# Kernel optimization log

Measured on AMD Instinct MI355X. Metric: run time of the kernel, lower is better.

## Reference

```python
import jax, jax.numpy as jnp
import numpy as np

B, T, N, H = 16, 49, 24, 256
S = 0.05  # init scale (keeps sigmoids/tanh out of saturation for numeric testing)


def setup_inputs() -> dict:
    key = jax.random.key(0)
    ks = jax.random.split(key, 16)
    rn = lambda k, shp: (jax.random.normal(k, shp, dtype=jnp.float32) * S)
    return dict(
        h=rn(ks[0], (B, T, N, H)),
        c_h=rn(ks[1], (B, T, N, H)),
        p=rn(ks[2], (B, T, N, H)),
        g_t=rn(ks[3], (B, T, N, H)),
        c_g_t=rn(ks[4], (B, T, N, H)),
        g_s=rn(ks[5], (B, T, N, H)),
        c_g_s=rn(ks[6], (B, T, N, H)),
        # 9 h-gates stacked in order: i, lt, ft, rt, s, gt, gs, o, c
        U=rn(ks[7], (9, N, H, H)),
        Wt=rn(ks[8], (9, N, 3 * H, H)),
        Ws=rn(ks[9], (9, N, H, H)),
        Zt=rn(ks[10], (9, N, H, H)),
        Zs=rn(ks[11], (9, N, H, H)),
        b=rn(ks[12], (9, N, 1, H)),
        # 6 global gates stacked in order: gtf, gtg, gto, gsf, gsg, gso
        Wg=rn(ks[13], (6, N, H, H)),
        Zg=rn(ks[14], (6, N, H, H)),
        bg=rn(ks[15], (6, N, 1, H)),
        train=1,
    )


def _cell(h, c_h, p, g_t, c_g_t, g_s, c_g_s, U, Wt, Ws, Zt, Zs, b, Wg, Zg, bg):
    pad_t = jnp.zeros_like(h[:, :, :1, :])
    pad_s = jnp.zeros_like(h[:, :1, :, :])
    # spatial (bone) neighbours along axis 2
    h_t_before = jnp.concatenate([pad_t, h[:, :, :-1, :]], axis=2)
    h_t_after = jnp.concatenate([h[:, :, 1:, :], pad_t], axis=2)
    h_tba = jnp.concatenate([h_t_before, h, h_t_after], axis=3)  # [B,T,N,3H]
    c_t_before = jnp.concatenate([pad_t, c_h[:, :, :-1, :]], axis=2)
    c_t_after = jnp.concatenate([c_h[:, :, 1:, :], pad_t], axis=2)
    # temporal predecessor along axis 1
    h_s_before = jnp.concatenate([pad_s, h[:, :-1, :, :]], axis=1)
    c_s_before = jnp.concatenate([pad_s, c_h[:, :-1, :, :]], axis=1)

    # Faithful quirk of the source: f_ft gate uses Zslt (the lt gate's Zs) for its g_s term.
    Zs_eff = Zs.at[2].set(Zs[1])

    # All 9 gate preactivations in one fused batched-GEMM pass: [9,B,T,N,H]
    pre = (jnp.einsum('btnh,gnhk->gbtnk', p, U)
           + jnp.einsum('btnm,gnmk->gbtnk', h_tba, Wt)
           + jnp.einsum('btnh,gnhk->gbtnk', h_s_before, Ws)
           + jnp.einsum('btnh,gnhk->gbtnk', g_t, Zt)
           + jnp.einsum('btnh,gnhk->gbtnk', g_s, Zs_eff)
           + b[:, None, None, :, 0, :])
    i_n, f_lt, f_ft, f_rt, f_s, f_gt, f_gs, o_n = jax.nn.sigmoid(pre[:8])
    c_n = jnp.tanh(pre[8])

    c_h_new = (f_lt * c_t_before + f_ft * c_h + f_rt * c_t_after
               + f_s * c_s_before + f_gt * c_g_t + f_gs * c_g_s + i_n * c_n)
    h_new = o_n * jnp.tanh(c_h_new)

    def _global(x_g, c_g, Wg3, Zg3, bg3):
        pre_g = (jnp.einsum('btnh,gnhk->gbtnk', h_new, Wg3)
                 + jnp.einsum('btnh,gnhk->gbtnk', x_g, Zg3)
                 + bg3[:, None, None, :, 0, :])
        f_g = jax.nn.sigmoid(pre_g[0])
        cand = jnp.tanh(pre_g[1])
        o_g = jax.nn.sigmoid(pre_g[2])
        c_g_new = f_g * c_g + (1.0 - f_g) * cand
        return o_g * jnp.tanh(c_g_new), c_g_new

    g_t_new, c_g_t_new = _global(g_t, c_g_t, Wg[:3], Zg[:3], bg[:3])
    g_s_new, c_g_s_new = _global(g_s, c_g_s, Wg[3:], Zg[3:], bg[3:])
    return h_new, c_h_new, g_t_new, c_g_t_new, g_s_new, c_g_s_new


def reference(h, c_h, p, g_t, c_g_t, g_s, c_g_s, U, Wt, Ws, Zt, Zs, b, Wg, Zg, bg, train):
    # `train` is a flag unused by the cell's math (kept for signature fidelity)
    return _cell(h, c_h, p, g_t, c_g_t, g_s, c_g_s, U, Wt, Ws, Zt, Zs, b, Wg, Zg, bg)
```

## Files before the change

### kernel.cpp

```cpp
#include <hip/hip_runtime.h>
#include <hip/hip_bf16.h>

typedef unsigned short u16;
typedef u16 u16x8 __attribute__((ext_vector_type(8)));
typedef short s16x8 __attribute__((ext_vector_type(8)));
typedef float f32x4 __attribute__((ext_vector_type(4)));
typedef unsigned int u32;

#define NN 24
#define TT 49
#define MR 784
#define SZT 4816896

__device__ inline u16 f2b(float f){
    __hip_bfloat16 b = __float2bfloat16(f); u16 r; __builtin_memcpy(&r, &b, 2); return r;
}
__device__ inline float sig_(float x){ return 1.f / (1.f + __expf(-x)); }
__device__ inline float tanh_(float x){ float e = __expf(2.f * x); return (e - 1.f) / (e + 1.f); }

__device__ inline void gld16(const u16* g, u16* l){
    __builtin_amdgcn_global_load_lds(
        (const __attribute__((address_space(1))) unsigned int*)g,
        (__attribute__((address_space(3))) unsigned int*)l, 16, 0, 0);
}

#define WT0_ELEMS ((size_t)216 * 256 * 1792)
#define WT1_ELEMS ((size_t)144 * 256 * 512)

__global__ __launch_bounds__(256) void wprep0(
    const float* __restrict__ U,  const float* __restrict__ Wt,
    const float* __restrict__ Ws, const float* __restrict__ Zt,
    const float* __restrict__ Zs, u16* __restrict__ out)
{
    __shared__ u16 T[64][72];
    const int tid = threadIdx.x;
    const int kt = blockIdx.x, ct = blockIdx.y, z = blockIdx.z;
    const int n = z % NN, g = z / NN;
    const int k0 = kt * 64;

    const float* wbase;
    if (k0 < 256)       wbase = U  + (size_t)((g * NN + n) * 256 + k0)          * 256;
    else if (k0 < 1024) wbase = Wt + (size_t)((g * NN + n) * 768 + (k0 - 256))  * 256;
    else if (k0 < 1280) wbase = Ws + (size_t)((g * NN + n) * 256 + (k0 - 1024)) * 256;
    else if (k0 < 1536) wbase = Zt + (size_t)((g * NN + n) * 256 + (k0 - 1280)) * 256;
    else { const int g2 = (g == 2) ? 1 : g;
           wbase = Zs + (size_t)((g2 * NN + n) * 256 + (k0 - 1536)) * 256; }

    const int colg = ct * 64 + (tid & 15) * 4;
    #pragma unroll
    for (int it = 0; it < 4; ++it) {
        const int krl = (tid >> 4) + it * 16;
        const float4 v = *(const float4*)(wbase + (size_t)krl * 256 + colg);
        const int cl = (tid & 15) * 4;
        T[cl + 0][krl] = f2b(v.x); T[cl + 1][krl] = f2b(v.y);
        T[cl + 2][krl] = f2b(v.z); T[cl + 3][krl] = f2b(v.w);
    }
    __syncthreads();
    const int col_l = tid >> 2, ks = (tid & 3) * 16;
    const int ktile = 2 * kt + (ks >> 5);
    const int koff  = ks & 31;
    u16* dst = out + (size_t)z * 458752 + (size_t)ktile * 8192
                   + (size_t)(ct * 64 + col_l) * 32 + koff;
    u16x8 w0, w1;
    #pragma unroll
    for (int j = 0; j < 8; ++j) { w0[j] = T[col_l][ks + j]; w1[j] = T[col_l][ks + 8 + j]; }
    *(u16x8*)(dst) = w0; *(u16x8*)(dst + 8) = w1;
}

__global__ __launch_bounds__(256) void wprep1(
    const float* __restrict__ Wg, const float* __restrict__ Zg, u16* __restrict__ out)
{
    __shared__ u16 T[64][72];
    const int tid = threadIdx.x;
    const int kt = blockIdx.x, ct = blockIdx.y, z = blockIdx.z;
    const int k0 = kt * 64;
    const float* wbase = (k0 < 256)
        ? Wg + (size_t)(z * 256 + k0) * 256
        : Zg + (size_t)(z * 256 + (k0 - 256)) * 256;

    const int colg = ct * 64 + (tid & 15) * 4;
    #pragma unroll
    for (int it = 0; it < 4; ++it) {
        const int krl = (tid >> 4) + it * 16;
        const float4 v = *(const float4*)(wbase + (size_t)krl * 256 + colg);
        const int cl = (tid & 15) * 4;
        T[cl + 0][krl] = f2b(v.x); T[cl + 1][krl] = f2b(v.y);
        T[cl + 2][krl] = f2b(v.z); T[cl + 3][krl] = f2b(v.w);
    }
    __syncthreads();
    const int col_l = tid >> 2, ks = (tid & 3) * 16;
    const int ktile = 2 * kt + (ks >> 5);
    const int koff  = ks & 31;
    u16* dst = out + (size_t)z * 131072 + (size_t)ktile * 8192
                   + (size_t)(ct * 64 + col_l) * 32 + koff;
    u16x8 w0, w1;
    #pragma unroll
    for (int j = 0; j < 8; ++j) { w0[j] = T[col_l][ks + j]; w1[j] = T[col_l][ks + 8 + j]; }
    *(u16x8*)(dst) = w0; *(u16x8*)(dst + 8) = w1;
}

#define AB2 2048
#define BB2 18432

__global__ __launch_bounds__(256, 2) void fused_cell4(
    const float* __restrict__ p,   const float* __restrict__ h,
    const float* __restrict__ c_h, const float* __restrict__ g_t,
    const float* __restrict__ c_g_t, const float* __restrict__ g_s,
    const float* __restrict__ c_g_s,
    const u16* __restrict__ WT0, const float* __restrict__ Bias,
    float* __restrict__ h_new, float* __restrict__ c_h_new)
{
    extern __shared__ u16 smem[];

    const int tid = threadIdx.x;
    const int lin = blockIdx.x;
    const int xcd = lin & 7, j = lin >> 3;
    const int mtile = j % 13;
    const int slab  = (j / 13) * 8 + xcd;
    const int ntile = slab & 3, n = slab >> 2;

    const int s_r = tid >> 2, s_c = tid & 3;
    const int gr  = mtile * 64 + s_r;
    const bool mval = (gr < MR);
    const int ec = (gr * NN + n) * 256;
    const bool vnb = (n > 0), vna = (n < NN - 1), vtp = (gr % TT) != 0;

    const int wro = s_r * 32 + ((s_c ^ ((s_r >> 1) & 3)) << 3);

    const int wave = tid >> 6, lane = tid & 63;
    const int lrow = lane & 15, lci = lane >> 4;

    int aro[4];
    #pragma unroll
    for (int m = 0; m < 4; ++m) {
        const int row = m * 16 + lrow;
        aro[m] = row * 32 + ((lci ^ ((row >> 1) & 3)) << 3);
    }
    const int colr = wave * 16 + lrow;
    const int bro  = colr * 32 + ((lci ^ ((colr >> 1) & 3)) << 3);

    const size_t bsrc = (size_t)(ntile * 64) * 32 + (size_t)wro;
    const u16* wbase = WT0 + (size_t)n * 458752 + bsrc;

    f32x4 acc[9][4];
    #pragma unroll
    for (int g = 0; g < 9; ++g)
        #pragma unroll
        for (int m = 0; m < 4; ++m) acc[g][m] = f32x4{0.f, 0.f, 0.f, 0.f};

    float4 alo, ahi;

    auto loadA = [&](int kt) {
        const int K0 = kt * 32, seg = K0 >> 8, koff = (K0 & 255) + s_c * 8;
        const float* src = nullptr; bool valid = mval;
        switch (seg) {
            case 0: src = p + ec + koff; break;
            case 1: valid &= vnb; src = h + ec - 256 + koff; break;
            case 2: src = h + ec + koff; break;
            case 3: valid &= vna; src = h + ec + 256 + koff; break;
            case 4: valid &= vtp; src = h + ec - NN * 256 + koff; break;
            case 5: src = g_t + ec + koff; break;
            default: src = g_s + ec + koff; break;
        }
        alo = make_float4(0.f, 0.f, 0.f, 0.f); ahi = alo;
        if (valid) { alo = *(const float4*)src; ahi = *(const float4*)(src + 4); }
    };
    auto storeA = [&](int buf) {
        u16x8 aw;
        aw[0] = f2b(alo.x); aw[1] = f2b(alo.y); aw[2] = f2b(alo.z); aw[3] = f2b(alo.w);
        aw[4] = f2b(ahi.x); aw[5] = f2b(ahi.y); aw[6] = f2b(ahi.z); aw[7] = f2b(ahi.w);
        *(u16x8*)(&smem[buf * AB2 + wro]) = aw;
    };
    auto dmaB = [&](int kt, int buf) {
        const u16* wb = wbase + (size_t)kt * 8192;
        u16* dst = &smem[2 * AB2 + buf * BB2 + tid * 8];
        #pragma unroll
        for (int g = 0; g < 9; ++g)
            gld16(wb + (size_t)g * 11010048, dst + g * 2048);
    };
    auto domfma = [&](int buf) {
        const u16* Asb = smem + buf * AB2;
        const u16* Bsb = smem + 2 * AB2 + buf * BB2;
        s16x8 af[4];
        #pragma unroll
        for (int m = 0; m < 4; ++m) af[m] = *(const s16x8*)(&Asb[aro[m]]);
        __builtin_amdgcn_s_setprio(1);
        #pragma unroll
        for (int g = 0; g < 9; ++g) {
            const s16x8 bf = *(const s16x8*)(&Bsb[g * 2048 + bro]);
            #pragma unroll
            for (int m = 0; m < 4; ++m)
                acc[g][m] = __builtin_amdgcn_mfma_f32_16x16x32_bf16(af[m], bf, acc[g][m], 0, 0, 0);
        }
        __builtin_amdgcn_s_setprio(0);
    };

    dmaB(0, 0); loadA(0); storeA(0);
    for (int kt = 0; kt < 56; kt += 2) {
        __syncthreads();
        dmaB(kt + 1, 1); loadA(kt + 1);
        domfma(0);
        storeA(1);
        __syncthreads();
        if (kt + 2 < 56) { dmaB(kt + 2, 0); loadA(kt + 2); }
        domfma(1);
        if (kt + 2 < 56) storeA(0);
    }

    const int col = ntile * 64 + wave * 16 + lrow;
    float bv[9];
    #pragma unroll
    for (int g = 0; g < 9; ++g) bv[g] = Bias[(g * NN + n) * 256 + col];

    #pragma unroll
    for (int m = 0; m < 4; ++m) {
        #pragma unroll
        for (int i = 0; i < 4; ++i) {
            const int row = mtile * 64 + m * 16 + (lane >> 4) * 4 + i;
            if (row < MR) {
                const size_t e = ((size_t)(row * NN + n)) * 256 + col;
                const float i_n  = sig_(acc[0][m][i] + bv[0]);
                const float f_lt = sig_(acc[1][m][i] + bv[1]);
                const float f_ft = sig_(acc[2][m][i] + bv[2]);
                const float f_rt = sig_(acc[3][m][i] + bv[3]);
                const float f_s  = sig_(acc[4][m][i] + bv[4]);
                const float f_gt = sig_(acc[5][m][i] + bv[5]);
                const float f_gs = sig_(acc[6][m][i] + bv[6]);
                const float o_n  = sig_(acc[7][m][i] + bv[7]);
                const float c_n  = tanh_(acc[8][m][i] + bv[8]);
                const float cb = (n > 0)      ? c_h[e - 256] : 0.f;
                const float ca = (n < NN - 1) ? c_h[e + 256] : 0.f;
                const float cs = (row % TT)   ? c_h[e - NN * 256] : 0.f;
                const float cn = f_lt * cb + f_ft * c_h[e] + f_rt * ca
                               + f_s * cs + f_gt * c_g_t[e] + f_gs * c_g_s[e]
                               + i_n * c_n;
                c_h_new[e] = cn;
                h_new[e]   = o_n * tanh_(cn);
            }
        }
    }
}

__global__ __launch_bounds__(256, 4) void fused_global4(
    const float* __restrict__ hn,   const float* __restrict__ g_t,
    const float* __restrict__ g_s,  const float* __restrict__ c_g_t,
    const float* __restrict__ c_g_s,
    const u16* __restrict__ WT1, const float* __restrict__ Bg,
    float* __restrict__ out2, float* __restrict__ out3,
    float* __restrict__ out4, float* __restrict__ out5)
{
    __shared__ u16 smem[2 * 2048 + 2 * 6144];

    const int tid = threadIdx.x;
    const int lin = blockIdx.x;
    const int xcd = lin & 7, j = lin >> 3;
    const int mtile = j % 13;
    const int slab  = (j / 13) * 8 + xcd;
    const int ntile = slab & 3;
    const int zz    = slab >> 2;
    const int n = zz % NN, grp = zz / NN;

    const float* xg = grp ? g_s : g_t;
    const float* cg = grp ? c_g_s : c_g_t;
    float* og  = grp ? out4 : out2;
    float* ocg = grp ? out5 : out3;

    const int s_r = tid >> 2, s_c = tid & 3;
    const int gr  = mtile * 64 + s_r;
    const bool mval = (gr < MR);
    const int ec = (gr * NN + n) * 256;

    const int wro = s_r * 32 + ((s_c ^ ((s_r >> 1) & 3)) << 3);

    const int wave = tid >> 6, lane = tid & 63;
    const int lrow = lane & 15, lci = lane >> 4;

    int aro[4];
    #pragma unroll
    for (int m = 0; m < 4; ++m) {
        const int row = m * 16 + lrow;
        aro[m] = row * 32 + ((lci ^ ((row >> 1) & 3)) << 3);
    }
    const int colr = wave * 16 + lrow;
    const int bro  = colr * 32 + ((lci ^ ((colr >> 1) & 3)) << 3);

    const size_t bsrc = (size_t)(ntile * 64) * 32 + (size_t)wro;
    const u16* wbase = WT1 + (size_t)(grp * 3 * NN + n) * 131072 + bsrc;

    f32x4 acc[3][4];
    #pragma unroll
    for (int g = 0; g < 3; ++g)
        #pragma unroll
        for (int m = 0; m < 4; ++m) acc[g][m] = f32x4{0.f, 0.f, 0.f, 0.f};

    float4 alo, ahi;

    auto loadA = [&](int kt) {
        const int K0 = kt * 32, koff = (K0 & 255) + s_c * 8;
        const float* src = ((K0 < 256) ? hn : xg) + ec + koff;
        alo = make_float4(0.f, 0.f, 0.f, 0.f); ahi = alo;
        if (mval) { alo = *(const float4*)src; ahi = *(const float4*)(src + 4); }
    };
    auto storeA = [&](int buf) {
        u16x8 aw;
        aw[0] = f2b(alo.x); aw[1] = f2b(alo.y); aw[2] = f2b(alo.z); aw[3] = f2b(alo.w);
        aw[4] = f2b(ahi.x); aw[5] = f2b(ahi.y); aw[6] = f2b(ahi.z); aw[7] = f2b(ahi.w);
        *(u16x8*)(&smem[buf * 2048 + wro]) = aw;
    };
    auto dmaB = [&](int kt, int buf) {
        const u16* wb = wbase + (size_t)kt * 8192;
        u16* dst = &smem[2 * 2048 + buf * 6144 + tid * 8];
        #pragma unroll
        for (int g = 0; g < 3; ++g)
            gld16(wb + (size_t)g * 3145728, dst + g * 2048);
    };
    auto domfma = [&](int buf) {
        const u16* Asb = smem + buf * 2048;
        const u16* Bsb = smem + 2 * 2048 + buf * 6144;
        s16x8 af[4];
        #pragma unroll
        for (int m = 0; m < 4; ++m) af[m] = *(const s16x8*)(&Asb[aro[m]]);
        __builtin_amdgcn_s_setprio(1);
        #pragma unroll
        for (int g = 0; g < 3; ++g) {
            const s16x8 bf = *(const s16x8*)(&Bsb[g * 2048 + bro]);
            #pragma unroll
            for (int m = 0; m < 4; ++m)
                acc[g][m] = __builtin_amdgcn_mfma_f32_16x16x32_bf16(af[m], bf, acc[g][m], 0, 0, 0);
        }
        __builtin_amdgcn_s_setprio(0);
    };

    dmaB(0, 0); loadA(0); storeA(0);
    for (int kt = 0; kt < 16; kt += 2) {
        __syncthreads();
        dmaB(kt + 1, 1); loadA(kt + 1);
        domfma(0);
        storeA(1);
        __syncthreads();
        if (kt + 2 < 16) { dmaB(kt + 2, 0); loadA(kt + 2); }
        domfma(1);
        if (kt + 2 < 16) storeA(0);
    }

    const int col = ntile * 64 + wave * 16 + lrow;
    float bv[3];
    #pragma unroll
    for (int g = 0; g < 3; ++g) bv[g] = Bg[((grp * 3 + g) * NN + n) * 256 + col];

    #pragma unroll
    for (int m = 0; m < 4; ++m) {
        #pragma unroll
        for (int i = 0; i < 4; ++i) {
            const int row = mtile * 64 + m * 16 + (lane >> 4) * 4 + i;
            if (row < MR) {
                const size_t e = ((size_t)(row * NN + n)) * 256 + col;
                const float f    = sig_(acc[0][m][i] + bv[0]);
                const float cand = tanh_(acc[1][m][i] + bv[1]);
                const float o    = sig_(acc[2][m][i] + bv[2]);
                const float cn = f * cg[e] + (1.f - f) * cand;
                ocg[e] = cn;
                og[e]  = o * tanh_(cn);
            }
        }
    }
}

extern "C" void kernel_launch(void* const* d_in, const int* in_sizes, int n_in,
                              void* d_out, int out_size, void* d_ws, size_t ws_size,
                              hipStream_t stream)
{
    const float* h     = (const float*)d_in[0];
    const float* c_h   = (const float*)d_in[1];
    const float* p     = (const float*)d_in[2];
    const float* g_t   = (const float*)d_in[3];
    const float* c_g_t = (const float*)d_in[4];
    const float* g_s   = (const float*)d_in[5];
    const float* c_g_s = (const float*)d_in[6];
    const float* U     = (const float*)d_in[7];
    const float* Wt    = (const float*)d_in[8];
    const float* Ws    = (const float*)d_in[9];
    const float* Zt    = (const float*)d_in[10];
    const float* Zs    = (const float*)d_in[11];
    const float* bb    = (const float*)d_in[12];
    const float* Wg    = (const float*)d_in[13];
    const float* Zg    = (const float*)d_in[14];
    const float* bg    = (const float*)d_in[15];

    float* out0 = (float*)d_out;
    float* out1 = out0 + (size_t)SZT;
    float* out2 = out1 + (size_t)SZT;
    float* out3 = out2 + (size_t)SZT;
    float* out4 = out3 + (size_t)SZT;
    float* out5 = out4 + (size_t)SZT;

    u16* wt0 = (u16*)d_ws;
    u16* wt1 = wt0 + WT0_ELEMS;

    dim3 blk(256);
    wprep0<<<dim3(28, 4, 216), blk, 0, stream>>>(U, Wt, Ws, Zt, Zs, wt0);
    wprep1<<<dim3(8, 4, 144), blk, 0, stream>>>(Wg, Zg, wt1);

    hipFuncSetAttribute((const void*)fused_cell4,
                        hipFuncAttributeMaxDynamicSharedMemorySize, 81920);
    fused_cell4<<<dim3(1248), blk, 81920, stream>>>(
        p, h, c_h, g_t, c_g_t, g_s, c_g_s, wt0, bb, out0, out1);
    fused_global4<<<dim3(2496), blk, 0, stream>>>(
        out0, g_t, g_s, c_g_t, c_g_s, wt1, bg, out2, out3, out4, out5);
}
```

Baseline: 487.9 us.

## Pre-pack activations to bf16 tiles and DMA them directly into LDS

Adds an aprep kernel that gathers the seven concatenated activation segments (p, h neighbours, temporal predecessor, g_t, g_s), converts them to bf16 and writes them in a tile-major layout in the workspace. A new fused_cell5 then streams these A tiles into LDS with global_load_lds, as it already does for weights. This removes the per-tile fp32 loads, conversions and LDS stores from the GEMM main loop, and cuts the A traffic that was reloaded once per column tile. It costs an extra pass that writes and reads a ~34MB bf16 buffer, and it only runs when the workspace is large enough; otherwise the old kernel runs with loads reordered.

```diff
diff --git a/kernel.cpp b/kernel.cpp
--- a/kernel.cpp
+++ b/kernel.cpp
@@ -26,6 +26,9 @@
 
 #define WT0_ELEMS ((size_t)216 * 256 * 1792)
 #define WT1_ELEMS ((size_t)144 * 256 * 512)
+#define ABF_ELEMS ((size_t)24 * 56 * 784 * 32)
+#define NEED_BASE ((WT0_ELEMS + WT1_ELEMS) * 2)
+#define NEED_A    (NEED_BASE + ABF_ELEMS * 2 + 4096)
 
 __global__ __launch_bounds__(256) void wprep0(
     const float* __restrict__ U,  const float* __restrict__ Wt,
@@ -99,15 +102,45 @@
     *(u16x8*)(dst) = w0; *(u16x8*)(dst + 8) = w1;
 }
 
+__global__ __launch_bounds__(256) void aprep(
+    const float* __restrict__ p,   const float* __restrict__ h,
+    const float* __restrict__ g_t, const float* __restrict__ g_s,
+    u16* __restrict__ Abf)
+{
+    const int tid = threadIdx.x;
+    const int bx = blockIdx.x, kt = blockIdx.y, n = blockIdx.z;
+    const int row = bx * 64 + (tid >> 2);
+    if (row >= MR) return;
+    const int c  = tid & 3;
+    const int kg = kt * 32 + c * 8;
+    const int seg = kg >> 8, koff = kg & 255;
+    const int ec = (row * NN + n) * 256 + koff;
+    const float* src = nullptr; bool valid = true;
+    switch (seg) {
+        case 0: src = p + ec; break;
+        case 1: valid = (n > 0);          src = h + ec - 256; break;
+        case 2: src = h + ec; break;
+        case 3: valid = (n < NN - 1);     src = h + ec + 256; break;
+        case 4: valid = (row % TT) != 0;  src = h + ec - NN * 256; break;
+        case 5: src = g_t + ec; break;
+        default: src = g_s + ec; break;
+    }
+    float4 lo = {0.f,0.f,0.f,0.f}, hi = lo;
+    if (valid) { lo = *(const float4*)src; hi = *(const float4*)(src + 4); }
+    u16x8 w;
+    w[0] = f2b(lo.x); w[1] = f2b(lo.y); w[2] = f2b(lo.z); w[3] = f2b(lo.w);
+    w[4] = f2b(hi.x); w[5] = f2b(hi.y); w[6] = f2b(hi.z); w[7] = f2b(hi.w);
+    *(u16x8*)(Abf + ((size_t)(n * 56 + kt) * MR + row) * 32 + c * 8) = w;
+}
+
 #define AB2 2048
 #define BB2 18432
 
-__global__ __launch_bounds__(256, 2) void fused_cell4(
-    const float* __restrict__ p,   const float* __restrict__ h,
-    const float* __restrict__ c_h, const float* __restrict__ g_t,
-    const float* __restrict__ c_g_t, const float* __restrict__ g_s,
+__global__ __launch_bounds__(256, 2) void fused_cell5(
+    const float* __restrict__ c_h, const float* __restrict__ c_g_t,
     const float* __restrict__ c_g_s,
-    const u16* __restrict__ WT0, const float* __restrict__ Bias,
+    const u16* __restrict__ Abf, const u16* __restrict__ WT0,
+    const float* __restrict__ Bias,
     float* __restrict__ h_new, float* __restrict__ c_h_new)
 {
     extern __shared__ u16 smem[];
@@ -120,11 +153,6 @@
     const int ntile = slab & 3, n = slab >> 2;
 
     const int s_r = tid >> 2, s_c = tid & 3;
-    const int gr  = mtile * 64 + s_r;
-    const bool mval = (gr < MR);
-    const int ec = (gr * NN + n) * 256;
-    const bool vnb = (n > 0), vna = (n < NN - 1), vtp = (gr % TT) != 0;
-
     const int wro = s_r * 32 + ((s_c ^ ((s_r >> 1) & 3)) << 3);
 
     const int wave = tid >> 6, lane = tid & 63;
@@ -139,8 +167,8 @@
     const int colr = wave * 16 + lrow;
     const int bro  = colr * 32 + ((lci ^ ((colr >> 1) & 3)) << 3);
 
-    const size_t bsrc = (size_t)(ntile * 64) * 32 + (size_t)wro;
-    const u16* wbase = WT0 + (size_t)n * 458752 + bsrc;
+    const u16* abase = Abf + ((size_t)(n * 56) * MR + mtile * 64) * 32 + wro;
+    const u16* wbase = WT0 + (size_t)n * 458752 + (size_t)(ntile * 64) * 32 + wro;
 
     f32x4 acc[9][4];
     #pragma unroll
@@ -148,30 +176,8 @@
         #pragma unroll
         for (int m = 0; m < 4; ++m) acc[g][m] = f32x4{0.f, 0.f, 0.f, 0.f};
 
-    float4 alo, ahi;
-
-    auto loadA = [&](int kt) {
-        const int K0 = kt * 32, seg = K0 >> 8, koff = (K0 & 255) + s_c * 8;
-        const float* src = nullptr; bool valid = mval;
-        switch (seg) {
-            case 0: src = p + ec + koff; break;
-            case 1: valid &= vnb; src = h + ec - 256 + koff; break;
-            case 2: src = h + ec + koff; break;
-            case 3: valid &= vna; src = h + ec + 256 + koff; break;
-            case 4: valid &= vtp; src = h + ec - NN * 256 + koff; break;
-            case 5: src = g_t + ec + koff; break;
-            default: src = g_s + ec + koff; break;
-        }
-        alo = make_float4(0.f, 0.f, 0.f, 0.f); ahi = alo;
-        if (valid) { alo = *(const float4*)src; ahi = *(const float4*)(src + 4); }
-    };
-    auto storeA = [&](int buf) {
-        u16x8 aw;
-        aw[0] = f2b(alo.x); aw[1] = f2b(alo.y); aw[2] = f2b(alo.z); aw[3] = f2b(alo.w);
-        aw[4] = f2b(ahi.x); aw[5] = f2b(ahi.y); aw[6] = f2b(ahi.z); aw[7] = f2b(ahi.w);
-        *(u16x8*)(&smem[buf * AB2 + wro]) = aw;
-    };
-    auto dmaB = [&](int kt, int buf) {
+    auto dma = [&](int kt, int buf) {
+        gld16(abase + (size_t)kt * (MR * 32), &smem[buf * AB2 + tid * 8]);
         const u16* wb = wbase + (size_t)kt * 8192;
         u16* dst = &smem[2 * AB2 + buf * BB2 + tid * 8];
         #pragma unroll
@@ -195,16 +201,14 @@
         __builtin_amdgcn_s_setprio(0);
     };
 
-    dmaB(0, 0); loadA(0); storeA(0);
+    dma(0, 0);
     for (int kt = 0; kt < 56; kt += 2) {
         __syncthreads();
-        dmaB(kt + 1, 1); loadA(kt + 1);
+        dma(kt + 1, 1);
         domfma(0);
-        storeA(1);
         __syncthreads();
-        if (kt + 2 < 56) { dmaB(kt + 2, 0); loadA(kt + 2); }
+        if (kt + 2 < 56) dma(kt + 2, 0);
         domfma(1);
-        if (kt + 2 < 56) storeA(0);
     }
 
     const int col = ntile * 64 + wave * 16 + lrow;
@@ -241,6 +245,145 @@
     }
 }
 
+__global__ __launch_bounds__(256, 2) void fused_cell4(
+    const float* __restrict__ p,   const float* __restrict__ h,
+    const float* __restrict__ c_h, const float* __restrict__ g_t,
+    const float* __restrict__ c_g_t, const float* __restrict__ g_s,
+    const float* __restrict__ c_g_s,
+    const u16* __restrict__ WT0, const float* __restrict__ Bias,
+    float* __restrict__ h_new, float* __restrict__ c_h_new)
+{
+    extern __shared__ u16 smem[];
+
+    const int tid = threadIdx.x;
+    const int lin = blockIdx.x;
+    const int xcd = lin & 7, j = lin >> 3;
+    const int mtile = j % 13;
+    const int slab  = (j / 13) * 8 + xcd;
+    const int ntile = slab & 3, n = slab >> 2;
+
+    const int s_r = tid >> 2, s_c = tid & 3;
+    const int gr  = mtile * 64 + s_r;
+    const bool mval = (gr < MR);
+    const int ec = (gr * NN + n) * 256;
+    const bool vnb = (n > 0), vna = (n < NN - 1), vtp = (gr % TT) != 0;
+
+    const int wro = s_r * 32 + ((s_c ^ ((s_r >> 1) & 3)) << 3);
+
+    const int wave = tid >> 6, lane = tid & 63;
+    const int lrow = lane & 15, lci = lane >> 4;
+
+    int aro[4];
+    #pragma unroll
+    for (int m = 0; m < 4; ++m) {
+        const int row = m * 16 + lrow;
+        aro[m] = row * 32 + ((lci ^ ((row >> 1) & 3)) << 3);
+    }
+    const int colr = wave * 16 + lrow;
+    const int bro  = colr * 32 + ((lci ^ ((colr >> 1) & 3)) << 3);
+
+    const size_t bsrc = (size_t)(ntile * 64) * 32 + (size_t)wro;
+    const u16* wbase = WT0 + (size_t)n * 458752 + bsrc;
+
+    f32x4 acc[9][4];
+    #pragma unroll
+    for (int g = 0; g < 9; ++g)
+        #pragma unroll
+        for (int m = 0; m < 4; ++m) acc[g][m] = f32x4{0.f, 0.f, 0.f, 0.f};
+
+    float4 alo, ahi;
+
+    auto loadA = [&](int kt) {
+        const int K0 = kt * 32, seg = K0 >> 8, koff = (K0 & 255) + s_c * 8;
+        const float* src = nullptr; bool valid = mval;
+        switch (seg) {
+            case 0: src = p + ec + koff; break;
+            case 1: valid &= vnb; src = h + ec - 256 + koff; break;
+            case 2: src = h + ec + koff; break;
+            case 3: valid &= vna; src = h + ec + 256 + koff; break;
+            case 4: valid &= vtp; src = h + ec - NN * 256 + koff; break;
+            case 5: src = g_t + ec + koff; break;
+            default: src = g_s + ec + koff; break;
+        }
+        alo = make_float4(0.f, 0.f, 0.f, 0.f); ahi = alo;
+        if (valid) { alo = *(const float4*)src; ahi = *(const float4*)(src + 4); }
+    };
+    auto storeA = [&](int buf) {
+        u16x8 aw;
+        aw[0] = f2b(alo.x); aw[1] = f2b(alo.y); aw[2] = f2b(alo.z); aw[3] = f2b(alo.w);
+        aw[4] = f2b(ahi.x); aw[5] = f2b(ahi.y); aw[6] = f2b(ahi.z); aw[7] = f2b(ahi.w);
+        *(u16x8*)(&smem[buf * AB2 + wro]) = aw;
+    };
+    auto dmaB = [&](int kt, int buf) {
+        const u16* wb = wbase + (size_t)kt * 8192;
+        u16* dst = &smem[2 * AB2 + buf * BB2 + tid * 8];
+        #pragma unroll
+        for (int g = 0; g < 9; ++g)
+            gld16(wb + (size_t)g * 11010048, dst + g * 2048);
+    };
+    auto domfma = [&](int buf) {
+        const u16* Asb = smem + buf * AB2;
+        const u16* Bsb = smem + 2 * AB2 + buf * BB2;
+        s16x8 af[4];
+        #pragma unroll
+        for (int m = 0; m < 4; ++m) af[m] = *(const s16x8*)(&Asb[aro[m]]);
+        __builtin_amdgcn_s_setprio(1);
+        #pragma unroll
+        for (int g = 0; g < 9; ++g) {
+            const s16x8 bf = *(const s16x8*)(&Bsb[g * 2048 + bro]);
+            #pragma unroll
+            for (int m = 0; m < 4; ++m)
+                acc[g][m] = __builtin_amdgcn_mfma_f32_16x16x32_bf16(af[m], bf, acc[g][m], 0, 0, 0);
+        }
+        __builtin_amdgcn_s_setprio(0);
+    };
+
+    dmaB(0, 0); loadA(0); storeA(0);
+    for (int kt = 0; kt < 56; kt += 2) {
+        __syncthreads();
+        loadA(kt + 1); dmaB(kt + 1, 1);
+        domfma(0);
+        storeA(1);
+        __syncthreads();
+        if (kt + 2 < 56) { loadA(kt + 2); dmaB(kt + 2, 0); }
+        domfma(1);
+        if (kt + 2 < 56) storeA(0);
+    }
+
+    const int col = ntile * 64 + wave * 16 + lrow;
+    float bv[9];
+    #pragma unroll
+    for (int g = 0; g < 9; ++g) bv[g] = Bias[(g * NN + n) * 256 + col];
+
+    #pragma unroll
+    for (int m = 0; m < 4; ++m) {
+        #pragma unroll
+        for (int i = 0; i < 4; ++i) {
+            const int row = mtile * 64 + m * 16 + (lane >> 4) * 4 + i;
+            if (row < MR) {
+                const size_t e = ((size_t)(row * NN + n)) * 256 + col;
+                const float i_n  = sig_(acc[0][m][i] + bv[0]);
+                const float f_lt = sig_(acc[1][m][i] + bv[1]);
+                const float f_ft = sig_(acc[2][m][i] + bv[2]);
+                const float f_rt = sig_(acc[3][m][i] + bv[3]);
+                const float f_s  = sig_(acc[4][m][i] + bv[4]);
+                const float f_gt = sig_(acc[5][m][i] + bv[5]);
+                const float f_gs = sig_(acc[6][m][i] + bv[6]);
+                const float o_n  = sig_(acc[7][m][i] + bv[7]);
+                const float c_n  = tanh_(acc[8][m][i] + bv[8]);
+                const float cb = (n > 0)      ? c_h[e - 256] : 0.f;
+                const float ca = (n < NN - 1) ? c_h[e + 256] : 0.f;
+                const float cs = (row % TT)   ? c_h[e - NN * 256] : 0.f;
+                const float cn = f_lt * cb + f_ft * c_h[e] + f_rt * ca
+                               + f_s * cs + f_gt * c_g_t[e] + f_gs * c_g_s[e]
+                               + i_n * c_n;
+                c_h_new[e] = cn;
+                h_new[e]   = o_n * tanh_(cn);
+            }
+        }
+    }
+}
+
 __global__ __launch_bounds__(256, 4) void fused_global4(
     const float* __restrict__ hn,   const float* __restrict__ g_t,
     const float* __restrict__ g_s,  const float* __restrict__ c_g_t,
@@ -331,14 +474,14 @@
         __builtin_amdgcn_s_setprio(0);
     };
 
-    dmaB(0, 0); loadA(0); storeA(0);
+    loadA(0); dmaB(0, 0); storeA(0);
     for (int kt = 0; kt < 16; kt += 2) {
         __syncthreads();
-        dmaB(kt + 1, 1); loadA(kt + 1);
+        loadA(kt + 1); dmaB(kt + 1, 1);
         domfma(0);
         storeA(1);
         __syncthreads();
-        if (kt + 2 < 16) { dmaB(kt + 2, 0); loadA(kt + 2); }
+        if (kt + 2 < 16) { loadA(kt + 2); dmaB(kt + 2, 0); }
         domfma(1);
         if (kt + 2 < 16) storeA(0);
     }
@@ -396,15 +539,24 @@
 
     u16* wt0 = (u16*)d_ws;
     u16* wt1 = wt0 + WT0_ELEMS;
+    u16* abf = wt1 + WT1_ELEMS;
 
     dim3 blk(256);
     wprep0<<<dim3(28, 4, 216), blk, 0, stream>>>(U, Wt, Ws, Zt, Zs, wt0);
     wprep1<<<dim3(8, 4, 144), blk, 0, stream>>>(Wg, Zg, wt1);
 
-    hipFuncSetAttribute((const void*)fused_cell4,
-                        hipFuncAttributeMaxDynamicSharedMemorySize, 81920);
-    fused_cell4<<<dim3(1248), blk, 81920, stream>>>(
-        p, h, c_h, g_t, c_g_t, g_s, c_g_s, wt0, bb, out0, out1);
+    if (ws_size >= NEED_A) {
+        aprep<<<dim3(13, 56, 24), blk, 0, stream>>>(p, h, g_t, g_s, abf);
+        hipFuncSetAttribute((const void*)fused_cell5,
+                            hipFuncAttributeMaxDynamicSharedMemorySize, 81920);
+        fused_cell5<<<dim3(1248), blk, 81920, stream>>>(
+            c_h, c_g_t, c_g_s, abf, wt0, bb, out0, out1);
+    } else {
+        hipFuncSetAttribute((const void*)fused_cell4,
+                            hipFuncAttributeMaxDynamicSharedMemorySize, 81920);
+        fused_cell4<<<dim3(1248), blk, 81920, stream>>>(
+            p, h, c_h, g_t, c_g_t, g_s, c_g_s, wt0, bb, out0, out1);
+    }
     fused_global4<<<dim3(2496), blk, 0, stream>>>(
         out0, g_t, g_s, c_g_t, c_g_s, wt1, bg, out2, out3, out4, out5);
 }
```

Measured after the change: 512.4 us. +5.0%, slower.

## Pre-convert activations to bf16 tiles and DMA both operands with explicit waitcnt pipelining

Applied to the files above, without the earlier changes.

The two weight-prep kernels are merged into one prep launch, which also converts the concatenated A operand (p, h neighbours, g_t, g_s) into a bf16 k-tiled buffer in workspace. The main cell GEMM then loads A straight into LDS with global_load_lds alongside B, so the fp32-load, convert and LDS-store work leaves its inner loop. Its loop is restructured around raw s_barrier and vmcnt waits so the next tile's DMA overlaps the current MFMA. The global-gate kernel gets a similar double-register prefetch with explicit waitcnts. In exchange, an extra bf16 activation buffer has to be written and read back, and the hand-tuned waitcnt counts add a correctness risk.

```diff
diff --git a/kernel.cpp b/kernel.cpp
--- a/kernel.cpp
+++ b/kernel.cpp
@@ -24,90 +24,118 @@
         (__attribute__((address_space(3))) unsigned int*)l, 16, 0, 0);
 }
 
+#define BAR()      __builtin_amdgcn_s_barrier()
+#define WAITVM(N)  asm volatile("s_waitcnt vmcnt(" #N ")" ::: "memory")
+#define WAITVL(N)  asm volatile("s_waitcnt vmcnt(" #N ") lgkmcnt(0)" ::: "memory")
+
 #define WT0_ELEMS ((size_t)216 * 256 * 1792)
 #define WT1_ELEMS ((size_t)144 * 256 * 512)
 
-__global__ __launch_bounds__(256) void wprep0(
+__global__ __launch_bounds__(256) void prep_all(
     const float* __restrict__ U,  const float* __restrict__ Wt,
     const float* __restrict__ Ws, const float* __restrict__ Zt,
-    const float* __restrict__ Zs, u16* __restrict__ out)
+    const float* __restrict__ Zs, const float* __restrict__ Wg,
+    const float* __restrict__ Zg,
+    const float* __restrict__ p,  const float* __restrict__ h,
+    const float* __restrict__ g_t, const float* __restrict__ g_s,
+    u16* __restrict__ wt0, u16* __restrict__ wt1, u16* __restrict__ Abf)
 {
     __shared__ u16 T[64][72];
     const int tid = threadIdx.x;
-    const int kt = blockIdx.x, ct = blockIdx.y, z = blockIdx.z;
-    const int n = z % NN, g = z / NN;
-    const int k0 = kt * 64;
-
-    const float* wbase;
-    if (k0 < 256)       wbase = U  + (size_t)((g * NN + n) * 256 + k0)          * 256;
-    else if (k0 < 1024) wbase = Wt + (size_t)((g * NN + n) * 768 + (k0 - 256))  * 256;
-    else if (k0 < 1280) wbase = Ws + (size_t)((g * NN + n) * 256 + (k0 - 1024)) * 256;
-    else if (k0 < 1536) wbase = Zt + (size_t)((g * NN + n) * 256 + (k0 - 1280)) * 256;
-    else { const int g2 = (g == 2) ? 1 : g;
-           wbase = Zs + (size_t)((g2 * NN + n) * 256 + (k0 - 1536)) * 256; }
-
-    const int colg = ct * 64 + (tid & 15) * 4;
-    #pragma unroll
-    for (int it = 0; it < 4; ++it) {
-        const int krl = (tid >> 4) + it * 16;
-        const float4 v = *(const float4*)(wbase + (size_t)krl * 256 + colg);
-        const int cl = (tid & 15) * 4;
-        T[cl + 0][krl] = f2b(v.x); T[cl + 1][krl] = f2b(v.y);
-        T[cl + 2][krl] = f2b(v.z); T[cl + 3][krl] = f2b(v.w);
-    }
-    __syncthreads();
-    const int col_l = tid >> 2, ks = (tid & 3) * 16;
-    const int ktile = 2 * kt + (ks >> 5);
-    const int koff  = ks & 31;
-    u16* dst = out + (size_t)z * 458752 + (size_t)ktile * 8192
-                   + (size_t)(ct * 64 + col_l) * 32 + koff;
-    u16x8 w0, w1;
-    #pragma unroll
-    for (int j = 0; j < 8; ++j) { w0[j] = T[col_l][ks + j]; w1[j] = T[col_l][ks + 8 + j]; }
-    *(u16x8*)(dst) = w0; *(u16x8*)(dst + 8) = w1;
-}
-
-__global__ __launch_bounds__(256) void wprep1(
-    const float* __restrict__ Wg, const float* __restrict__ Zg, u16* __restrict__ out)
-{
-    __shared__ u16 T[64][72];
-    const int tid = threadIdx.x;
-    const int kt = blockIdx.x, ct = blockIdx.y, z = blockIdx.z;
-    const int k0 = kt * 64;
-    const float* wbase = (k0 < 256)
-        ? Wg + (size_t)(z * 256 + k0) * 256
-        : Zg + (size_t)(z * 256 + (k0 - 256)) * 256;
-
-    const int colg = ct * 64 + (tid & 15) * 4;
-    #pragma unroll
-    for (int it = 0; it < 4; ++it) {
-        const int krl = (tid >> 4) + it * 16;
-        const float4 v = *(const float4*)(wbase + (size_t)krl * 256 + colg);
-        const int cl = (tid & 15) * 4;
-        T[cl + 0][krl] = f2b(v.x); T[cl + 1][krl] = f2b(v.y);
-        T[cl + 2][krl] = f2b(v.z); T[cl + 3][krl] = f2b(v.w);
-    }
-    __syncthreads();
-    const int col_l = tid >> 2, ks = (tid & 3) * 16;
-    const int ktile = 2 * kt + (ks >> 5);
-    const int koff  = ks & 31;
-    u16* dst = out + (size_t)z * 131072 + (size_t)ktile * 8192
-                   + (size_t)(ct * 64 + col_l) * 32 + koff;
-    u16x8 w0, w1;
-    #pragma unroll
-    for (int j = 0; j < 8; ++j) { w0[j] = T[col_l][ks + j]; w1[j] = T[col_l][ks + 8 + j]; }
-    *(u16x8*)(dst) = w0; *(u16x8*)(dst + 8) = w1;
+    const int lin = blockIdx.x;
+
+    if (lin < 24192) {
+        const int kt = lin % 28, ct = (lin / 28) % 4, z = lin / 112;
+        const int n = z % NN, g = z / NN;
+        const int k0 = kt * 64;
+        const float* wbase;
+        if (k0 < 256)       wbase = U  + (size_t)((g * NN + n) * 256 + k0)          * 256;
+        else if (k0 < 1024) wbase = Wt + (size_t)((g * NN + n) * 768 + (k0 - 256))  * 256;
+        else if (k0 < 1280) wbase = Ws + (size_t)((g * NN + n) * 256 + (k0 - 1024)) * 256;
+        else if (k0 < 1536) wbase = Zt + (size_t)((g * NN + n) * 256 + (k0 - 1280)) * 256;
+        else { const int g2 = (g == 2) ? 1 : g;
+               wbase = Zs + (size_t)((g2 * NN + n) * 256 + (k0 - 1536)) * 256; }
+        const int colg = ct * 64 + (tid & 15) * 4;
+        #pragma unroll
+        for (int it = 0; it < 4; ++it) {
+            const int krl = (tid >> 4) + it * 16;
+            const float4 v = *(const float4*)(wbase + (size_t)krl * 256 + colg);
+            const int cl = (tid & 15) * 4;
+            T[cl + 0][krl] = f2b(v.x); T[cl + 1][krl] = f2b(v.y);
+            T[cl + 2][krl] = f2b(v.z); T[cl + 3][krl] = f2b(v.w);
+        }
+        __syncthreads();
+        const int col_l = tid >> 2, ks = (tid & 3) * 16;
+        const int ktile = 2 * kt + (ks >> 5);
+        const int koff  = ks & 31;
+        u16* dst = wt0 + (size_t)z * 458752 + (size_t)ktile * 8192
+                       + (size_t)(ct * 64 + col_l) * 32 + koff;
+        u16x8 w0, w1;
+        #pragma unroll
+        for (int j2 = 0; j2 < 8; ++j2) { w0[j2] = T[col_l][ks + j2]; w1[j2] = T[col_l][ks + 8 + j2]; }
+        *(u16x8*)(dst) = w0; *(u16x8*)(dst + 8) = w1;
+    } else if (lin < 28800) {
+        const int l = lin - 24192;
+        const int kt = l % 8, ct = (l / 8) % 4, z = l / 32;
+        const int k0 = kt * 64;
+        const float* wbase = (k0 < 256)
+            ? Wg + (size_t)(z * 256 + k0) * 256
+            : Zg + (size_t)(z * 256 + (k0 - 256)) * 256;
+        const int colg = ct * 64 + (tid & 15) * 4;
+        #pragma unroll
+        for (int it = 0; it < 4; ++it) {
+            const int krl = (tid >> 4) + it * 16;
+            const float4 v = *(const float4*)(wbase + (size_t)krl * 256 + colg);
+            const int cl = (tid & 15) * 4;
+            T[cl + 0][krl] = f2b(v.x); T[cl + 1][krl] = f2b(v.y);
+            T[cl + 2][krl] = f2b(v.z); T[cl + 3][krl] = f2b(v.w);
+        }
+        __syncthreads();
+        const int col_l = tid >> 2, ks = (tid & 3) * 16;
+        const int ktile = 2 * kt + (ks >> 5);
+        const int koff  = ks & 31;
+        u16* dst = wt1 + (size_t)z * 131072 + (size_t)ktile * 8192
+                       + (size_t)(ct * 64 + col_l) * 32 + koff;
+        u16x8 w0, w1;
+        #pragma unroll
+        for (int j2 = 0; j2 < 8; ++j2) { w0[j2] = T[col_l][ks + j2]; w1[j2] = T[col_l][ks + 8 + j2]; }
+        *(u16x8*)(dst) = w0; *(u16x8*)(dst + 8) = w1;
+    } else {
+        const int l = lin - 28800;
+        const int bx = l % 13, kt = (l / 13) % 56, n = l / 728;
+        const int row = bx * 64 + (tid >> 2);
+        if (row >= MR) return;
+        const int c  = tid & 3;
+        const int kg = kt * 32 + c * 8;
+        const int seg = kg >> 8, koff = kg & 255;
+        const int ec = (row * NN + n) * 256 + koff;
+        const float* src = nullptr; bool valid = true;
+        switch (seg) {
+            case 0: src = p + ec; break;
+            case 1: valid = (n > 0);          src = h + ec - 256; break;
+            case 2: src = h + ec; break;
+            case 3: valid = (n < NN - 1);     src = h + ec + 256; break;
+            case 4: valid = (row % TT) != 0;  src = h + ec - NN * 256; break;
+            case 5: src = g_t + ec; break;
+            default: src = g_s + ec; break;
+        }
+        float4 lo = {0.f,0.f,0.f,0.f}, hi = lo;
+        if (valid) { lo = *(const float4*)src; hi = *(const float4*)(src + 4); }
+        u16x8 w;
+        w[0] = f2b(lo.x); w[1] = f2b(lo.y); w[2] = f2b(lo.z); w[3] = f2b(lo.w);
+        w[4] = f2b(hi.x); w[5] = f2b(hi.y); w[6] = f2b(hi.z); w[7] = f2b(hi.w);
+        *(u16x8*)(Abf + ((size_t)(n * 56 + kt) * MR + row) * 32 + c * 8) = w;
+    }
 }
 
 #define AB2 2048
 #define BB2 18432
 
-__global__ __launch_bounds__(256, 2) void fused_cell4(
-    const float* __restrict__ p,   const float* __restrict__ h,
-    const float* __restrict__ c_h, const float* __restrict__ g_t,
-    const float* __restrict__ c_g_t, const float* __restrict__ g_s,
+__global__ __launch_bounds__(256, 2) void fused_cell6(
+    const float* __restrict__ c_h, const float* __restrict__ c_g_t,
     const float* __restrict__ c_g_s,
-    const u16* __restrict__ WT0, const float* __restrict__ Bias,
+    const u16* __restrict__ Abf, const u16* __restrict__ WT0,
+    const float* __restrict__ Bias,
     float* __restrict__ h_new, float* __restrict__ c_h_new)
 {
     extern __shared__ u16 smem[];
@@ -120,11 +148,6 @@
     const int ntile = slab & 3, n = slab >> 2;
 
     const int s_r = tid >> 2, s_c = tid & 3;
-    const int gr  = mtile * 64 + s_r;
-    const bool mval = (gr < MR);
-    const int ec = (gr * NN + n) * 256;
-    const bool vnb = (n > 0), vna = (n < NN - 1), vtp = (gr % TT) != 0;
-
     const int wro = s_r * 32 + ((s_c ^ ((s_r >> 1) & 3)) << 3);
 
     const int wave = tid >> 6, lane = tid & 63;
@@ -139,8 +162,8 @@
     const int colr = wave * 16 + lrow;
     const int bro  = colr * 32 + ((lci ^ ((colr >> 1) & 3)) << 3);
 
-    const size_t bsrc = (size_t)(ntile * 64) * 32 + (size_t)wro;
-    const u16* wbase = WT0 + (size_t)n * 458752 + bsrc;
+    const u16* abase = Abf + ((size_t)(n * 56) * MR + mtile * 64) * 32 + wro;
+    const u16* wbase = WT0 + (size_t)n * 458752 + (size_t)(ntile * 64) * 32 + wro;
 
     f32x4 acc[9][4];
     #pragma unroll
@@ -148,30 +171,8 @@
         #pragma unroll
         for (int m = 0; m < 4; ++m) acc[g][m] = f32x4{0.f, 0.f, 0.f, 0.f};
 
-    float4 alo, ahi;
-
-    auto loadA = [&](int kt) {
-        const int K0 = kt * 32, seg = K0 >> 8, koff = (K0 & 255) + s_c * 8;
-        const float* src = nullptr; bool valid = mval;
-        switch (seg) {
-            case 0: src = p + ec + koff; break;
-            case 1: valid &= vnb; src = h + ec - 256 + koff; break;
-            case 2: src = h + ec + koff; break;
-            case 3: valid &= vna; src = h + ec + 256 + koff; break;
-            case 4: valid &= vtp; src = h + ec - NN * 256 + koff; break;
-            case 5: src = g_t + ec + koff; break;
-            default: src = g_s + ec + koff; break;
-        }
-        alo = make_float4(0.f, 0.f, 0.f, 0.f); ahi = alo;
-        if (valid) { alo = *(const float4*)src; ahi = *(const float4*)(src + 4); }
-    };
-    auto storeA = [&](int buf) {
-        u16x8 aw;
-        aw[0] = f2b(alo.x); aw[1] = f2b(alo.y); aw[2] = f2b(alo.z); aw[3] = f2b(alo.w);
-        aw[4] = f2b(ahi.x); aw[5] = f2b(ahi.y); aw[6] = f2b(ahi.z); aw[7] = f2b(ahi.w);
-        *(u16x8*)(&smem[buf * AB2 + wro]) = aw;
-    };
-    auto dmaB = [&](int kt, int buf) {
+    auto dma = [&](int kt, int buf) {
+        gld16(abase + (size_t)kt * (MR * 32), &smem[buf * AB2 + tid * 8]);
         const u16* wb = wbase + (size_t)kt * 8192;
         u16* dst = &smem[2 * AB2 + buf * BB2 + tid * 8];
         #pragma unroll
@@ -195,17 +196,23 @@
         __builtin_amdgcn_s_setprio(0);
     };
 
-    dmaB(0, 0); loadA(0); storeA(0);
-    for (int kt = 0; kt < 56; kt += 2) {
-        __syncthreads();
-        dmaB(kt + 1, 1); loadA(kt + 1);
+    dma(0, 0);
+    WAITVM(0); BAR();
+    dma(1, 1);
+    for (int kt = 0; kt < 54; kt += 2) {
         domfma(0);
-        storeA(1);
-        __syncthreads();
-        if (kt + 2 < 56) { dmaB(kt + 2, 0); loadA(kt + 2); }
+        BAR();
+        dma(kt + 2, 0);
+        WAITVM(10); BAR();
         domfma(1);
-        if (kt + 2 < 56) storeA(0);
-    }
+        BAR();
+        dma(kt + 3, 1);
+        WAITVM(10); BAR();
+    }
+    domfma(0);
+    BAR();
+    WAITVM(0); BAR();
+    domfma(1);
 
     const int col = ntile * 64 + wave * 16 + lrow;
     float bv[9];
@@ -241,7 +248,7 @@
     }
 }
 
-__global__ __launch_bounds__(256, 4) void fused_global4(
+__global__ __launch_bounds__(256, 4) void fused_global5(
     const float* __restrict__ hn,   const float* __restrict__ g_t,
     const float* __restrict__ g_s,  const float* __restrict__ c_g_t,
     const float* __restrict__ c_g_s,
@@ -284,8 +291,8 @@
     const int colr = wave * 16 + lrow;
     const int bro  = colr * 32 + ((lci ^ ((colr >> 1) & 3)) << 3);
 
-    const size_t bsrc = (size_t)(ntile * 64) * 32 + (size_t)wro;
-    const u16* wbase = WT1 + (size_t)(grp * 3 * NN + n) * 131072 + bsrc;
+    const u16* wbase = WT1 + (size_t)(grp * 3 * NN + n) * 131072
+                           + (size_t)(ntile * 64) * 32 + wro;
 
     f32x4 acc[3][4];
     #pragma unroll
@@ -293,18 +300,18 @@
         #pragma unroll
         for (int m = 0; m < 4; ++m) acc[g][m] = f32x4{0.f, 0.f, 0.f, 0.f};
 
-    float4 alo, ahi;
-
-    auto loadA = [&](int kt) {
+    float4 aOlo, aOhi, aNlo, aNhi;
+
+    auto loadA = [&](int kt, float4& lo, float4& hi) {
         const int K0 = kt * 32, koff = (K0 & 255) + s_c * 8;
         const float* src = ((K0 < 256) ? hn : xg) + ec + koff;
-        alo = make_float4(0.f, 0.f, 0.f, 0.f); ahi = alo;
-        if (mval) { alo = *(const float4*)src; ahi = *(const float4*)(src + 4); }
-    };
-    auto storeA = [&](int buf) {
+        lo = make_float4(0.f, 0.f, 0.f, 0.f); hi = lo;
+        if (mval) { lo = *(const float4*)src; hi = *(const float4*)(src + 4); }
+    };
+    auto storeA = [&](int buf, const float4& lo, const float4& hi) {
         u16x8 aw;
-        aw[0] = f2b(alo.x); aw[1] = f2b(alo.y); aw[2] = f2b(alo.z); aw[3] = f2b(alo.w);
-        aw[4] = f2b(ahi.x); aw[5] = f2b(ahi.y); aw[6] = f2b(ahi.z); aw[7] = f2b(ahi.w);
+        aw[0] = f2b(lo.x); aw[1] = f2b(lo.y); aw[2] = f2b(lo.z); aw[3] = f2b(lo.w);
+        aw[4] = f2b(hi.x); aw[5] = f2b(hi.y); aw[6] = f2b(hi.z); aw[7] = f2b(hi.w);
         *(u16x8*)(&smem[buf * 2048 + wro]) = aw;
     };
     auto dmaB = [&](int kt, int buf) {
@@ -331,17 +338,31 @@
         __builtin_amdgcn_s_setprio(0);
     };
 
-    dmaB(0, 0); loadA(0); storeA(0);
-    for (int kt = 0; kt < 16; kt += 2) {
-        __syncthreads();
-        dmaB(kt + 1, 1); loadA(kt + 1);
+    loadA(0, aOlo, aOhi);
+    dmaB(0, 0);
+    storeA(0, aOlo, aOhi);
+    loadA(1, aOlo, aOhi);
+    dmaB(1, 1);
+    WAITVL(5); BAR();
+    for (int kt = 0; kt < 14; kt += 2) {
         domfma(0);
-        storeA(1);
-        __syncthreads();
-        if (kt + 2 < 16) { dmaB(kt + 2, 0); loadA(kt + 2); }
+        BAR();
+        loadA(kt + 2, aNlo, aNhi);
+        dmaB(kt + 2, 0);
+        storeA(1, aOlo, aOhi);
+        WAITVL(5); BAR();
         domfma(1);
-        if (kt + 2 < 16) storeA(0);
-    }
+        BAR();
+        loadA(kt + 3, aOlo, aOhi);
+        dmaB(kt + 3, 1);
+        storeA(0, aNlo, aNhi);
+        WAITVL(5); BAR();
+    }
+    domfma(0);
+    BAR();
+    storeA(1, aOlo, aOhi);
+    WAITVL(0); BAR();
+    domfma(1);
 
     const int col = ntile * 64 + wave * 16 + lrow;
     float bv[3];
@@ -396,15 +417,16 @@
 
     u16* wt0 = (u16*)d_ws;
     u16* wt1 = wt0 + WT0_ELEMS;
+    u16* abf = wt1 + WT1_ELEMS;
 
     dim3 blk(256);
-    wprep0<<<dim3(28, 4, 216), blk, 0, stream>>>(U, Wt, Ws, Zt, Zs, wt0);
-    wprep1<<<dim3(8, 4, 144), blk, 0, stream>>>(Wg, Zg, wt1);
-
-    hipFuncSetAttribute((const void*)fused_cell4,
+    prep_all<<<dim3(46272), blk, 0, stream>>>(U, Wt, Ws, Zt, Zs, Wg, Zg,
+                                              p, h, g_t, g_s, wt0, wt1, abf);
+
+    hipFuncSetAttribute((const void*)fused_cell6,
                         hipFuncAttributeMaxDynamicSharedMemorySize, 81920);
-    fused_cell4<<<dim3(1248), blk, 81920, stream>>>(
-        p, h, c_h, g_t, c_g_t, g_s, c_g_s, wt0, bb, out0, out1);
-    fused_global4<<<dim3(2496), blk, 0, stream>>>(
+    fused_cell6<<<dim3(1248), blk, 81920, stream>>>(
+        c_h, c_g_t, c_g_s, abf, wt0, bb, out0, out1);
+    fused_global5<<<dim3(2496), blk, 0, stream>>>(
         out0, g_t, g_s, c_g_t, c_g_s, wt1, bg, out2, out3, out4, out5);
 }
```

Measured after the change: 467.8 us. 4.1% less time.
